# Performance work log

Hardware: AMD Instinct MI355X
Metric: run time of the kernel (lower is better)

The kernel has to match this reference:

```python
import jax, jax.numpy as jnp
import numpy as np

N, K, D, H = 2048, 128, 768, 512


def setup_inputs() -> dict:
    key = jax.random.key(0)
    k1, k2, k3, k4, k5, k6 = jax.random.split(key, 6)
    image_feat = jax.random.normal(k1, (N, D), dtype=jnp.float32)
    text_feat = jax.random.normal(k2, (K, D), dtype=jnp.float32)
    # nn.Linear(2D, H): weight (H, 2D), bias (H); stored transposed for clean matmul
    W1 = jax.random.normal(k3, (2 * D, H), dtype=jnp.float32) * (1.0 / np.sqrt(2 * D))
    b1 = jax.random.normal(k4, (H,), dtype=jnp.float32) * 0.01
    # nn.Linear(H, 1)
    W2 = jax.random.normal(k5, (H, 1), dtype=jnp.float32) * (1.0 / np.sqrt(H))
    b2 = jax.random.normal(k6, (1,), dtype=jnp.float32) * 0.01
    return {"image_feat": image_feat, "text_feat": text_feat,
            "W1": W1, "b1": b1, "W2": W2, "b2": b2}


def reference(image_feat, text_feat, W1, b1, W2, b2):
    # concat([img, txt]) @ W1 == img @ W1[:D] + txt @ W1[D:]  (same math,
    # avoids materializing the (N,K,2D) concatenated tensor)
    img_proj = image_feat @ W1[:D]          # (N, H)
    txt_proj = text_feat @ W1[D:]           # (K, H)
    h = jax.nn.relu(img_proj[:, None, :] + txt_proj[None, :, :] + b1)  # (N, K, H)
    sim = (h @ W2).squeeze(-1) + b2[0]      # (N, K)
    return sim
```

## Files before the change

kernel.cpp:

```cpp
#include <hip/hip_runtime.h>
#include <hip/hip_bf16.h>

#define N_IMG 2048
#define K_TXT 128
#define D_IN  768
#define H_DIM 512
#define M_TOT (N_IMG + K_TXT)
#define NK    (N_IMG * K_TXT)
#define NTILE 16
#define NSLAB 4
#define HS    (H_DIM / NSLAB)

typedef __bf16 bf16x8 __attribute__((ext_vector_type(8)));
typedef float  f32x4  __attribute__((ext_vector_type(4)));
typedef float  f32x2  __attribute__((ext_vector_type(2)));

__global__ __launch_bounds__(256) void proj_kernel(
    const float* __restrict__ img, const float* __restrict__ txt,
    const float* __restrict__ W1, const float* __restrict__ b1,
    const float* __restrict__ W2, float* __restrict__ P,
    float* __restrict__ pw2)
{
    __shared__ __align__(16) __bf16 As[32][72];
    __shared__ __align__(16) __bf16 Bs[32][72];
    __shared__ float lds_pw[32];

    const int tid = threadIdx.x;
    const int n0 = (blockIdx.x & (NTILE - 1)) * 32;
    const int m0 = (blockIdx.x >> 4) * 32;
    const bool is_txt = (m0 >= N_IMG);
    const float* X  = is_txt ? (txt + (size_t)(m0 - N_IMG) * D_IN)
                             : (img + (size_t)m0 * D_IN);
    const float* Wb = W1 + (is_txt ? (size_t)D_IN * H_DIM : 0);

    const int wave = tid >> 6, lane = tid & 63;
    const int wm = (wave >> 1) * 16, wn = (wave & 1) * 16;
    const int quad = lane >> 4, lm = lane & 15;

    const int ar = tid >> 3, ak = (tid & 7) * 8;
    const int bn = tid & 31, bk = (tid >> 5) * 8;

    f32x4 acc = {0.f, 0.f, 0.f, 0.f};
    f32x4 aR0, aR1;
    float bR[8];

    auto loadA = [&](int kc) {
        const float* ap = X + (size_t)ar * D_IN + kc + ak;
        aR0 = *(const f32x4*)(ap + 0);
        aR1 = *(const f32x4*)(ap + 4);
    };
    auto loadB = [&](int kc) {
        #pragma unroll
        for (int j = 0; j < 8; ++j)
            bR[j] = Wb[(size_t)(kc + bk + j) * H_DIM + n0 + bn];
    };

    union BPack { __bf16 h[8]; uint4 u; };

    loadA(0); loadB(0);

    for (int it = 0; it < 12; ++it) {
        BPack pa;
        #pragma unroll
        for (int j = 0; j < 4; ++j) { pa.h[j] = (__bf16)aR0[j]; pa.h[4+j] = (__bf16)aR1[j]; }
        *(uint4*)&As[ar][ak] = pa.u;
        BPack q;
        #pragma unroll
        for (int j = 0; j < 8; ++j) q.h[j] = (__bf16)bR[j];
        *(uint4*)&Bs[bn][bk] = q.u;
        __syncthreads();

        if (it < 11) { loadA((it + 1) * 64); loadB((it + 1) * 64); }

        #pragma unroll
        for (int sub = 0; sub < 2; ++sub) {
            bf16x8 af = *(bf16x8*)&As[wm + lm][sub * 32 + quad * 8];
            bf16x8 bf = *(bf16x8*)&Bs[wn + lm][sub * 32 + quad * 8];
            acc = __builtin_amdgcn_mfma_f32_16x16x32_bf16(af, bf, acc, 0, 0, 0);
        }
        __syncthreads();
    }

    float rv[4];
    {
        const int gn = n0 + wn + lm;
        const float badd = is_txt ? b1[gn] : 0.0f;
        const float w2h = 0.5f * W2[gn];
        #pragma unroll
        for (int r = 0; r < 4; ++r) {
            const int gm = m0 + wm + quad * 4 + r;
            const float v = acc[r] + badd;
            P[(size_t)gm * H_DIM + gn] = v;
            rv[r] = v * w2h;
        }
    }
    #pragma unroll
    for (int m = 1; m < 16; m <<= 1) {
        #pragma unroll
        for (int r = 0; r < 4; ++r) rv[r] += __shfl_xor(rv[r], m, 64);
    }
    if (tid < 32) lds_pw[tid] = 0.f;
    __syncthreads();
    if (lm == 0) {
        #pragma unroll
        for (int r = 0; r < 4; ++r)
            atomicAdd(&lds_pw[wm + quad * 4 + r], rv[r]);
    }
    __syncthreads();
    if (tid < 32)
        pw2[(size_t)(blockIdx.x & (NTILE - 1)) * M_TOT + m0 + tid] = lds_pw[tid];
}

__global__ __launch_bounds__(256) void sim_kernel(
    const float* __restrict__ P, const float* __restrict__ W2,
    float* __restrict__ P2)
{
    __shared__ __align__(16) float Bs[32][HS];

    const int tid = threadIdx.x;
    const int n0 = blockIdx.x * 64;
    const int k0 = blockIdx.y * 32;
    const int hs = blockIdx.z;
    const int hc = hs * HS;

    #pragma unroll
    for (int i = 0; i < 4; ++i) {
        const int flat = tid + i * 256;
        const int row = flat >> 5, c4 = flat & 31;
        f32x4 v = *(const f32x4*)(P + (size_t)(N_IMG + k0 + row) * H_DIM + hc + c4 * 4);
        const int sc4 = c4 ^ ((row >> 1) & 7);
        *(f32x4*)&Bs[row][sc4 * 4] = v;
    }
    __syncthreads();

    const int tx = tid & 15;
    const int ty = tid >> 4;
    const int bswz = tx & 7;
    const int r0 = tx * 2;
    const float* pA = P + (size_t)(n0 + ty * 4) * H_DIM + hc;

    f32x2 acc[4];
    #pragma unroll
    for (int nn = 0; nn < 4; ++nn) acc[nn] = f32x2{0.f, 0.f};

    #pragma unroll 4
    for (int h4 = 0; h4 < HS / 4; ++h4) {
        const int sc = (h4 ^ bswz) * 4;
        f32x4 w  = *(const f32x4*)(W2 + hc + h4 * 4);
        f32x4 b0 = *(f32x4*)&Bs[r0][sc];
        f32x4 b1 = *(f32x4*)&Bs[r0 + 1][sc];
        f32x4 a[4];
        #pragma unroll
        for (int nn = 0; nn < 4; ++nn)
            a[nn] = *(const f32x4*)(pA + (size_t)nn * H_DIM + h4 * 4);

        #pragma unroll
        for (int nn = 0; nn < 4; ++nn) {
            #pragma unroll
            for (int hh = 0; hh < 4; ++hh) {
                const float t0 = a[nn][hh] + b0[hh];
                acc[nn][0] = fmaf(fabsf(t0), w[hh], acc[nn][0]);
                const float t1 = a[nn][hh] + b1[hh];
                acc[nn][1] = fmaf(fabsf(t1), w[hh], acc[nn][1]);
            }
        }
    }

    float* o = P2 + (size_t)hs * NK + (size_t)(n0 + ty * 4) * K_TXT + k0 + tx * 2;
    #pragma unroll
    for (int nn = 0; nn < 4; ++nn) {
        f32x2 st = { acc[nn][0] * 0.5f, acc[nn][1] * 0.5f };
        *(f32x2*)(o + (size_t)nn * K_TXT) = st;
    }
}

__global__ __launch_bounds__(256) void reduce_kernel(
    const float* __restrict__ P2, const float* __restrict__ pw2,
    const float* __restrict__ b2, float* __restrict__ out)
{
    __shared__ float pn_l[8];
    __shared__ __align__(16) float pk_l[K_TXT];

    const int tid = threadIdx.x;
    const int n0 = blockIdx.x * 8;

    if (tid < 8) {
        float s = 0.f;
        #pragma unroll
        for (int sl = 0; sl < NTILE; ++sl)
            s += pw2[(size_t)sl * M_TOT + n0 + tid];
        pn_l[tid] = s;
    } else if (tid >= 128) {
        const int k = tid - 128;
        float s = 0.f;
        #pragma unroll
        for (int sl = 0; sl < NTILE; ++sl)
            s += pw2[(size_t)sl * M_TOT + N_IMG + k];
        pk_l[k] = s;
    }
    __syncthreads();

    const int kq = tid & 31, nr = tid >> 5;
    const size_t base = (size_t)(n0 + nr) * K_TXT + kq * 4;

    f32x4 s = {0.f, 0.f, 0.f, 0.f};
    #pragma unroll
    for (int sl = 0; sl < NSLAB; ++sl)
        s += *(const f32x4*)(P2 + (size_t)sl * NK + base);

    const float add = pn_l[nr] + b2[0];
    f32x4 pk4 = *(f32x4*)&pk_l[kq * 4];
    s[0] += add + pk4[0]; s[1] += add + pk4[1];
    s[2] += add + pk4[2]; s[3] += add + pk4[3];
    *(f32x4*)(out + base) = s;
}

extern "C" void kernel_launch(void* const* d_in, const int* in_sizes, int n_in,
                              void* d_out, int out_size, void* d_ws, size_t ws_size,
                              hipStream_t stream) {
    const float* img = (const float*)d_in[0];
    const float* txt = (const float*)d_in[1];
    const float* W1  = (const float*)d_in[2];
    const float* b1  = (const float*)d_in[3];
    const float* W2  = (const float*)d_in[4];
    const float* b2  = (const float*)d_in[5];
    float* out = (float*)d_out;

    float* P   = (float*)d_ws;
    float* pw2 = P + (size_t)M_TOT * H_DIM;
    float* P2  = pw2 + (size_t)NTILE * M_TOT;

    proj_kernel  <<<dim3(68 * NTILE),                     256, 0, stream>>>(img, txt, W1, b1, W2, P, pw2);
    sim_kernel   <<<dim3(N_IMG / 64, K_TXT / 32, NSLAB),  256, 0, stream>>>(P, W2, P2);
    reduce_kernel<<<dim3(N_IMG / 8),                      256, 0, stream>>>(P2, pw2, b2, out);
}
```

Baseline: 100.2 us.

## Fuse reduction into sim kernel and split K across waves in projection GEMM

The similarity kernel now covers the full hidden dimension per block and writes the final output directly with the bias and rank-one terms added, so the separate reduce kernel and the slab partial buffer are gone. The projection kernel uses larger K chunks, with each wave handling a K slice for a full 32x32 tile and partials summed through LDS. This removes a launch and several MB of intermediate traffic. In exchange, the sim kernel launches half as many blocks and each uses a 64KB LDS tile, which may reduce occupancy.

```diff
diff --git a/kernel.cpp b/kernel.cpp
--- a/kernel.cpp
+++ b/kernel.cpp
@@ -8,12 +8,9 @@
 #define M_TOT (N_IMG + K_TXT)
 #define NK    (N_IMG * K_TXT)
 #define NTILE 16
-#define NSLAB 4
-#define HS    (H_DIM / NSLAB)
 
 typedef __bf16 bf16x8 __attribute__((ext_vector_type(8)));
 typedef float  f32x4  __attribute__((ext_vector_type(4)));
-typedef float  f32x2  __attribute__((ext_vector_type(2)));
 
 __global__ __launch_bounds__(256) void proj_kernel(
     const float* __restrict__ img, const float* __restrict__ txt,
@@ -21,9 +18,9 @@
     const float* __restrict__ W2, float* __restrict__ P,
     float* __restrict__ pw2)
 {
-    __shared__ __align__(16) __bf16 As[32][72];
-    __shared__ __align__(16) __bf16 Bs[32][72];
+    __shared__ __align__(16) __bf16 smem[2][32][136];
     __shared__ float lds_pw[32];
+    float* red = reinterpret_cast<float*>(&smem[0][0][0]);
 
     const int tid = threadIdx.x;
     const int n0 = (blockIdx.x & (NTILE - 1)) * 32;
@@ -34,78 +31,86 @@
     const float* Wb = W1 + (is_txt ? (size_t)D_IN * H_DIM : 0);
 
     const int wave = tid >> 6, lane = tid & 63;
-    const int wm = (wave >> 1) * 16, wn = (wave & 1) * 16;
     const int quad = lane >> 4, lm = lane & 15;
+    const int ksub = wave * 32;
 
-    const int ar = tid >> 3, ak = (tid & 7) * 8;
-    const int bn = tid & 31, bk = (tid >> 5) * 8;
+    const int ar = tid >> 3, ak = (tid & 7) * 16;
+    const int bn = tid & 31, bk = (tid >> 5) * 16;
 
-    f32x4 acc = {0.f, 0.f, 0.f, 0.f};
-    f32x4 aR0, aR1;
-    float bR[8];
+    f32x4 acc[2][2] = {};
+    f32x4 aR[4];
+    float bR[16];
 
     auto loadA = [&](int kc) {
         const float* ap = X + (size_t)ar * D_IN + kc + ak;
-        aR0 = *(const f32x4*)(ap + 0);
-        aR1 = *(const f32x4*)(ap + 4);
+        #pragma unroll
+        for (int j = 0; j < 4; ++j) aR[j] = *(const f32x4*)(ap + j * 4);
     };
     auto loadB = [&](int kc) {
         #pragma unroll
-        for (int j = 0; j < 8; ++j)
+        for (int j = 0; j < 16; ++j)
             bR[j] = Wb[(size_t)(kc + bk + j) * H_DIM + n0 + bn];
     };
 
-    union BPack { __bf16 h[8]; uint4 u; };
+    union Pack16 { __bf16 h[16]; uint4 u[2]; };
 
     loadA(0); loadB(0);
 
-    for (int it = 0; it < 12; ++it) {
-        BPack pa;
+    for (int it = 0; it < 6; ++it) {
+        Pack16 pa;
         #pragma unroll
-        for (int j = 0; j < 4; ++j) { pa.h[j] = (__bf16)aR0[j]; pa.h[4+j] = (__bf16)aR1[j]; }
-        *(uint4*)&As[ar][ak] = pa.u;
-        BPack q;
+        for (int j = 0; j < 4; ++j)
+            #pragma unroll
+            for (int c = 0; c < 4; ++c) pa.h[j * 4 + c] = (__bf16)aR[j][c];
+        *(uint4*)&smem[0][ar][ak]     = pa.u[0];
+        *(uint4*)&smem[0][ar][ak + 8] = pa.u[1];
+        Pack16 pb;
         #pragma unroll
-        for (int j = 0; j < 8; ++j) q.h[j] = (__bf16)bR[j];
-        *(uint4*)&Bs[bn][bk] = q.u;
+        for (int j = 0; j < 16; ++j) pb.h[j] = (__bf16)bR[j];
+        *(uint4*)&smem[1][bn][bk]     = pb.u[0];
+        *(uint4*)&smem[1][bn][bk + 8] = pb.u[1];
         __syncthreads();
 
-        if (it < 11) { loadA((it + 1) * 64); loadB((it + 1) * 64); }
+        if (it < 5) { loadA((it + 1) * 128); loadB((it + 1) * 128); }
 
-        #pragma unroll
-        for (int sub = 0; sub < 2; ++sub) {
-            bf16x8 af = *(bf16x8*)&As[wm + lm][sub * 32 + quad * 8];
-            bf16x8 bf = *(bf16x8*)&Bs[wn + lm][sub * 32 + quad * 8];
-            acc = __builtin_amdgcn_mfma_f32_16x16x32_bf16(af, bf, acc, 0, 0, 0);
-        }
+        bf16x8 af0 = *(bf16x8*)&smem[0][lm][ksub + quad * 8];
+        bf16x8 af1 = *(bf16x8*)&smem[0][16 + lm][ksub + quad * 8];
+        bf16x8 bf0 = *(bf16x8*)&smem[1][lm][ksub + quad * 8];
+        bf16x8 bf1 = *(bf16x8*)&smem[1][16 + lm][ksub + quad * 8];
+        acc[0][0] = __builtin_amdgcn_mfma_f32_16x16x32_bf16(af0, bf0, acc[0][0], 0, 0, 0);
+        acc[0][1] = __builtin_amdgcn_mfma_f32_16x16x32_bf16(af0, bf1, acc[0][1], 0, 0, 0);
+        acc[1][0] = __builtin_amdgcn_mfma_f32_16x16x32_bf16(af1, bf0, acc[1][0], 0, 0, 0);
+        acc[1][1] = __builtin_amdgcn_mfma_f32_16x16x32_bf16(af1, bf1, acc[1][1], 0, 0, 0);
         __syncthreads();
     }
 
-    float rv[4];
-    {
-        const int gn = n0 + wn + lm;
-        const float badd = is_txt ? b1[gn] : 0.0f;
-        const float w2h = 0.5f * W2[gn];
+    #pragma unroll
+    for (int mf = 0; mf < 2; ++mf)
         #pragma unroll
-        for (int r = 0; r < 4; ++r) {
-            const int gm = m0 + wm + quad * 4 + r;
-            const float v = acc[r] + badd;
-            P[(size_t)gm * H_DIM + gn] = v;
-            rv[r] = v * w2h;
-        }
-    }
+        for (int nf = 0; nf < 2; ++nf)
+            #pragma unroll
+            for (int r = 0; r < 4; ++r)
+                red[wave * 1024 + (mf * 16 + quad * 4 + r) * 32 + nf * 16 + lm]
+                    = acc[mf][nf][r];
+    __syncthreads();
+
+    const int orow = tid >> 3;
+    const int oc4  = (tid & 7) * 4;
+    f32x4 v = {};
     #pragma unroll
-    for (int m = 1; m < 16; m <<= 1) {
-        #pragma unroll
-        for (int r = 0; r < 4; ++r) rv[r] += __shfl_xor(rv[r], m, 64);
-    }
-    if (tid < 32) lds_pw[tid] = 0.f;
-    __syncthreads();
-    if (lm == 0) {
-        #pragma unroll
-        for (int r = 0; r < 4; ++r)
-            atomicAdd(&lds_pw[wm + quad * 4 + r], rv[r]);
-    }
+    for (int w = 0; w < 4; ++w)
+        v += *(f32x4*)&red[w * 1024 + orow * 32 + oc4];
+
+    const int gm = m0 + orow;
+    const int gn = n0 + oc4;
+    if (is_txt) v += *(const f32x4*)(b1 + gn);
+    *(f32x4*)&P[(size_t)gm * H_DIM + gn] = v;
+
+    f32x4 w2 = *(const f32x4*)(W2 + gn);
+    float rv = 0.5f * (v[0] * w2[0] + v[1] * w2[1] + v[2] * w2[2] + v[3] * w2[3]);
+    #pragma unroll
+    for (int m = 1; m < 8; m <<= 1) rv += __shfl_xor(rv, m, 64);
+    if ((tid & 7) == 0) lds_pw[orow] = rv;
     __syncthreads();
     if (tid < 32)
         pw2[(size_t)(blockIdx.x & (NTILE - 1)) * M_TOT + m0 + tid] = lds_pw[tid];
@@ -113,106 +118,65 @@
 
 __global__ __launch_bounds__(256) void sim_kernel(
     const float* __restrict__ P, const float* __restrict__ W2,
-    float* __restrict__ P2)
+    const float* __restrict__ pw2, const float* __restrict__ b2,
+    float* __restrict__ out)
 {
-    __shared__ __align__(16) float Bs[32][HS];
+    __shared__ __align__(16) float Bs[32][H_DIM];
+    __shared__ float pn_l[32], pk_l[32];
 
     const int tid = threadIdx.x;
-    const int n0 = blockIdx.x * 64;
+    const int n0 = blockIdx.x * 32;
     const int k0 = blockIdx.y * 32;
-    const int hs = blockIdx.z;
-    const int hc = hs * HS;
 
     #pragma unroll
-    for (int i = 0; i < 4; ++i) {
+    for (int i = 0; i < 16; ++i) {
         const int flat = tid + i * 256;
-        const int row = flat >> 5, c4 = flat & 31;
-        f32x4 v = *(const f32x4*)(P + (size_t)(N_IMG + k0 + row) * H_DIM + hc + c4 * 4);
-        const int sc4 = c4 ^ ((row >> 1) & 7);
-        *(f32x4*)&Bs[row][sc4 * 4] = v;
+        const int row = flat >> 7, c4 = flat & 127;
+        f32x4 v = *(const f32x4*)(P + (size_t)(N_IMG + k0 + row) * H_DIM + c4 * 4);
+        *(f32x4*)&Bs[row][(c4 ^ (row & 7)) * 4] = v;
     }
-    __syncthreads();
-
-    const int tx = tid & 15;
-    const int ty = tid >> 4;
-    const int bswz = tx & 7;
-    const int r0 = tx * 2;
-    const float* pA = P + (size_t)(n0 + ty * 4) * H_DIM + hc;
-
-    f32x2 acc[4];
-    #pragma unroll
-    for (int nn = 0; nn < 4; ++nn) acc[nn] = f32x2{0.f, 0.f};
-
-    #pragma unroll 4
-    for (int h4 = 0; h4 < HS / 4; ++h4) {
-        const int sc = (h4 ^ bswz) * 4;
-        f32x4 w  = *(const f32x4*)(W2 + hc + h4 * 4);
-        f32x4 b0 = *(f32x4*)&Bs[r0][sc];
-        f32x4 b1 = *(f32x4*)&Bs[r0 + 1][sc];
-        f32x4 a[4];
-        #pragma unroll
-        for (int nn = 0; nn < 4; ++nn)
-            a[nn] = *(const f32x4*)(pA + (size_t)nn * H_DIM + h4 * 4);
-
-        #pragma unroll
-        for (int nn = 0; nn < 4; ++nn) {
-            #pragma unroll
-            for (int hh = 0; hh < 4; ++hh) {
-                const float t0 = a[nn][hh] + b0[hh];
-                acc[nn][0] = fmaf(fabsf(t0), w[hh], acc[nn][0]);
-                const float t1 = a[nn][hh] + b1[hh];
-                acc[nn][1] = fmaf(fabsf(t1), w[hh], acc[nn][1]);
-            }
-        }
-    }
-
-    float* o = P2 + (size_t)hs * NK + (size_t)(n0 + ty * 4) * K_TXT + k0 + tx * 2;
-    #pragma unroll
-    for (int nn = 0; nn < 4; ++nn) {
-        f32x2 st = { acc[nn][0] * 0.5f, acc[nn][1] * 0.5f };
-        *(f32x2*)(o + (size_t)nn * K_TXT) = st;
-    }
-}
-
-__global__ __launch_bounds__(256) void reduce_kernel(
-    const float* __restrict__ P2, const float* __restrict__ pw2,
-    const float* __restrict__ b2, float* __restrict__ out)
-{
-    __shared__ float pn_l[8];
-    __shared__ __align__(16) float pk_l[K_TXT];
-
-    const int tid = threadIdx.x;
-    const int n0 = blockIdx.x * 8;
-
-    if (tid < 8) {
+    if (tid < 32) {
         float s = 0.f;
         #pragma unroll
         for (int sl = 0; sl < NTILE; ++sl)
             s += pw2[(size_t)sl * M_TOT + n0 + tid];
         pn_l[tid] = s;
-    } else if (tid >= 128) {
-        const int k = tid - 128;
+    } else if (tid < 64) {
+        const int k = tid - 32;
         float s = 0.f;
         #pragma unroll
         for (int sl = 0; sl < NTILE; ++sl)
-            s += pw2[(size_t)sl * M_TOT + N_IMG + k];
+            s += pw2[(size_t)sl * M_TOT + N_IMG + k0 + k];
         pk_l[k] = s;
     }
     __syncthreads();
 
-    const int kq = tid & 31, nr = tid >> 5;
-    const size_t base = (size_t)(n0 + nr) * K_TXT + kq * 4;
+    const int tx = tid & 31;
+    const int ty = tid >> 5;
+    const int sx = tx & 7;
+    const float* pA = P + (size_t)(n0 + ty * 4) * H_DIM;
 
-    f32x4 s = {0.f, 0.f, 0.f, 0.f};
+    f32x4 acc[4] = {};
+    #pragma unroll 8
+    for (int h4 = 0; h4 < H_DIM / 4; ++h4) {
+        f32x4 w = *(const f32x4*)(W2 + h4 * 4);
+        f32x4 b = *(f32x4*)&Bs[tx][(h4 ^ sx) * 4];
+        #pragma unroll
+        for (int nn = 0; nn < 4; ++nn) {
+            f32x4 a = *(const f32x4*)(pA + (size_t)nn * H_DIM + h4 * 4);
+            #pragma unroll
+            for (int hh = 0; hh < 4; ++hh)
+                acc[nn][hh] = fmaf(fabsf(a[hh] + b[hh]), w[hh], acc[nn][hh]);
+        }
+    }
+
+    const float addc = pk_l[tx] + b2[0];
     #pragma unroll
-    for (int sl = 0; sl < NSLAB; ++sl)
-        s += *(const f32x4*)(P2 + (size_t)sl * NK + base);
-
-    const float add = pn_l[nr] + b2[0];
-    f32x4 pk4 = *(f32x4*)&pk_l[kq * 4];
-    s[0] += add + pk4[0]; s[1] += add + pk4[1];
-    s[2] += add + pk4[2]; s[3] += add + pk4[3];
-    *(f32x4*)(out + base) = s;
+    for (int nn = 0; nn < 4; ++nn) {
+        const float s = (acc[nn][0] + acc[nn][1]) + (acc[nn][2] + acc[nn][3]);
+        out[(size_t)(n0 + ty * 4 + nn) * K_TXT + k0 + tx]
+            = 0.5f * s + pn_l[ty * 4 + nn] + addc;
+    }
 }
 
 extern "C" void kernel_launch(void* const* d_in, const int* in_sizes, int n_in,
@@ -228,9 +192,7 @@
 
     float* P   = (float*)d_ws;
     float* pw2 = P + (size_t)M_TOT * H_DIM;
-    float* P2  = pw2 + (size_t)NTILE * M_TOT;
 
-    proj_kernel  <<<dim3(68 * NTILE),                     256, 0, stream>>>(img, txt, W1, b1, W2, P, pw2);
-    sim_kernel   <<<dim3(N_IMG / 64, K_TXT / 32, NSLAB),  256, 0, stream>>>(P, W2, P2);
-    reduce_kernel<<<dim3(N_IMG / 8),                      256, 0, stream>>>(P2, pw2, b2, out);
+    proj_kernel<<<dim3(68 * NTILE),              256, 0, stream>>>(img, txt, W1, b1, W2, P, pw2);
+    sim_kernel <<<dim3(N_IMG / 32, K_TXT / 32),  256, 0, stream>>>(P, W2, pw2, b2, out);
 }
```

New measurement: 109.1 us. +8.9%, slower.
